# Kernel optimization log

Measured on AMD Instinct MI355X. Metric: run time of the kernel, lower is better.

## Reference

```python
import jax, jax.numpy as jnp
import numpy as np

LAYERS = 5      # lstm_layers
H = 1           # lstm_hidden_size
IN = 21         # 9 (rot) + 6 (v) + 6 (u)
NEG = 0.1       # LeakyReLU negative slope
EPS = 1e-5      # BatchNorm1d eps


def _lstm_cell(x, h, c, w_ih, w_hh):
    # torch gate order: i, f, g, o ; no biases (lstm_bias=False)
    gates = x @ w_ih.T + h @ w_hh.T              # [k, 4H]
    i, f, g, o = jnp.split(gates, 4, axis=-1)
    i = jax.nn.sigmoid(i)
    f = jax.nn.sigmoid(f)
    g = jnp.tanh(g)
    o = jax.nn.sigmoid(o)
    c_new = f * c + i * g
    h_new = o * jnp.tanh(c_new)
    return h_new, c_new


def _bn_train(z, gamma, beta):
    # BatchNorm1d in training mode: batch stats, biased variance
    m = z.mean(axis=0)
    var = z.var(axis=0)
    return gamma * (z - m) / jnp.sqrt(var + EPS) + beta


def setup_inputs() -> dict:
    key = jax.random.key(0)
    ks = jax.random.split(key, 14)
    k, T = 65536, 32
    s = 0.2  # init scale, roughly torch uniform(-1/sqrt(H)) magnitude
    inp = {
        "r": jax.random.normal(ks[0], (k, T, 9), jnp.float32),
        "v": jax.random.normal(ks[1], (k, T, 6), jnp.float32),
        "u": jax.random.normal(ks[2], (k, T, 6), jnp.float32),
        # LSTM weights: layer 0 sees IN features, layers 1..4 see H
        "w_ih0": jax.random.normal(ks[3], (4 * H, IN), jnp.float32) * s,
        "w_ih_rest": jax.random.normal(ks[4], (LAYERS - 1, 4 * H, H), jnp.float32) * s,
        "w_hh": jax.random.normal(ks[5], (LAYERS, 4 * H, H), jnp.float32) * s,
        # FC head: Linear(H,32,no bias) -> BN -> LReLU -> Linear(32,32) -> BN -> LReLU -> Linear(32,6)
        "W1": jax.random.normal(ks[6], (32, H), jnp.float32) * s,
        "g1": jnp.ones((32,), jnp.float32),
        "b1": jnp.zeros((32,), jnp.float32),
        "W2": jax.random.normal(ks[7], (32, 32), jnp.float32) * s,
        "g2": jnp.ones((32,), jnp.float32),
        "b2": jnp.zeros((32,), jnp.float32),
        "W3": jax.random.normal(ks[8], (6, 32), jnp.float32) * s,
    }
    return inp


def reference(r, v, u, w_ih0, w_ih_rest, w_hh, W1, g1, b1, W2, g2, b2, W3):
    x = jnp.concatenate([r, v, u], axis=-1)          # [k, T, 21]
    k = x.shape[0]
    h0 = jnp.zeros((LAYERS, k, H), x.dtype)
    c0 = jnp.zeros((LAYERS, k, H), x.dtype)
    xs = jnp.swapaxes(x, 0, 1)                       # [T, k, 21]

    def step(carry, xt):
        h, c = carry
        hs, cs = [], []
        layer_in = xt
        for l in range(LAYERS):
            w_ih = w_ih0 if l == 0 else w_ih_rest[l - 1]
            hl, cl = _lstm_cell(layer_in, h[l], c[l], w_ih, w_hh[l])
            hs.append(hl)
            cs.append(cl)
            layer_in = hl
        return (jnp.stack(hs), jnp.stack(cs)), layer_in  # top-layer output

    (hT, cT), outs = jax.lax.scan(step, (h0, c0), xs)    # outs: [T, k, H]

    # fc applied to out[:, 0] -> first timestep of top layer
    y = outs[0]                                          # [k, H]
    y = jax.nn.leaky_relu(_bn_train(y @ W1.T, g1, b1), NEG)
    y = jax.nn.leaky_relu(_bn_train(y @ W2.T, g2, b2), NEG)
    dv = y @ W3.T                                        # [k, 6]
    return dv[:, None], hT, cT
```

## Files before the change

### kernel.cpp

```cpp
#include <hip/hip_runtime.h>
#include <hip/hip_fp16.h>
#include <math.h>

#define T 32
#define NEGS 0.1f
#define EPS 1e-5f
#define NREG 33
#define NH (3 * NREG)


__device__ __forceinline__ float rcp_fast(float x) { return __builtin_amdgcn_rcpf(x); }
__device__ __forceinline__ float sigm(float x) { return rcp_fast(1.0f + __expf(-x)); }
__device__ __forceinline__ float tanh_fast(float x) {
    float t = __expf(2.0f * fabsf(x));
    float r = 1.0f - 2.0f * rcp_fast(t + 1.0f);
    return copysignf(r, x);
}
__device__ __forceinline__ float lrelu(float x) { return x > 0.0f ? x : NEGS * x; }

__device__ __forceinline__ void bn1_ab(const float* __restrict__ W1,
                                       const float* __restrict__ g1,
                                       const float* __restrict__ b1,
                                       float my, float vy, int j,
                                       float& a, float& b, float& tau, int& flip)
{
    float wj = W1[j];
    a = g1[j] * wj * rsqrtf(fmaf(wj * wj, vy, EPS));
    b = b1[j];
    if (a > 0.0f)      { tau = my - b / a; flip = 0; }
    else if (a < 0.0f) { tau = my - b / a; flip = 1; }
    else               { tau = (b > 0.0f ? -__builtin_inff() : __builtin_inff()); flip = 0; }
}

__device__ __forceinline__ void reduce_stats(const double* __restrict__ bSums, int nb, int k,
                                             float* outMy, float* outVy)
{
    const int tid = threadIdx.x;
    double sy = 0.0, sq = 0.0;
    for (int i = tid; i < nb; i += 256) { sy += bSums[2 * i]; sq += bSums[2 * i + 1]; }
#pragma unroll
    for (int off = 32; off; off >>= 1) {
        sy += __shfl_down(sy, off);
        sq += __shfl_down(sq, off);
    }
    __shared__ double dS[4], dQ[4];
    const int wid = tid >> 6, lane = tid & 63;
    if (lane == 0) { dS[wid] = sy; dQ[wid] = sq; }
    __syncthreads();
    if (tid == 0) {
        double tS = dS[0] + dS[1] + dS[2] + dS[3];
        double tQ = dQ[0] + dQ[1] + dQ[2] + dQ[3];
        float my = (float)(tS / k);
        *outMy = my;
        *outVy = (float)(tQ / k) - my * my;
    }
    __syncthreads();
}

__global__ __launch_bounds__(256)
void gates_kernel(const float* __restrict__ r, const float* __restrict__ v,
                  const float* __restrict__ u, const float* __restrict__ wih0,
                  ushort4* __restrict__ xg, int k)
{
    const int idx = blockIdx.x * 256 + threadIdx.x;
    const int s = idx >> 5, t = idx & 31;

    float wi0[4][21];
#pragma unroll
    for (int g = 0; g < 4; ++g)
#pragma unroll
        for (int j = 0; j < 21; ++j) wi0[g][j] = wih0[g * 21 + j];

    const float* rp = r + (size_t)s * 288 + t * 9;
    const float* vp = v + (size_t)s * 192 + t * 6;
    const float* up = u + (size_t)s * 192 + t * 6;
    float x[21];
#pragma unroll
    for (int j = 0; j < 9; ++j) x[j] = rp[j];
#pragma unroll
    for (int j = 0; j < 6; ++j) x[9 + j] = vp[j];
#pragma unroll
    for (int j = 0; j < 6; ++j) x[15 + j] = up[j];

    float acc[4];
#pragma unroll
    for (int g = 0; g < 4; ++g) {
        float a = 0.f;
#pragma unroll
        for (int j = 0; j < 21; ++j) a = fmaf(wi0[g][j], x[j], a);
        acc[g] = a;
    }
    ushort4 pk;
    pk.x = __half_as_ushort(__float2half(acc[0]));
    pk.y = __half_as_ushort(__float2half(acc[1]));
    pk.z = __half_as_ushort(__float2half(acc[2]));
    pk.w = __half_as_ushort(__float2half(acc[3]));
    xg[idx] = pk;
}

__global__ __launch_bounds__(256, 1)
void recur_kernel(const ushort4* __restrict__ xg, const float* __restrict__ wihr,
                  const float* __restrict__ whhp, float* __restrict__ out,
                  double* __restrict__ bSums, float* __restrict__ wsy, int k)
{
    const int s = blockIdx.x * 256 + threadIdx.x;

    float wir[4][4];
#pragma unroll
    for (int l = 0; l < 4; ++l)
#pragma unroll
        for (int g = 0; g < 4; ++g) wir[l][g] = wihr[l * 4 + g];
    float whh[5][4];
#pragma unroll
    for (int l = 0; l < 5; ++l)
#pragma unroll
        for (int g = 0; g < 4; ++g) whh[l][g] = whhp[l * 4 + g];

    ushort4 gbuf[T];
    const ushort4* gp = xg + (size_t)s * T;
#pragma unroll
    for (int t = 0; t < T; ++t) gbuf[t] = gp[t];

    float h[5] = {0.f, 0.f, 0.f, 0.f, 0.f};
    float c[5] = {0.f, 0.f, 0.f, 0.f, 0.f};
    float y0 = 0.f;

#pragma unroll
    for (int t = 0; t < T; ++t) {
        const ushort4 G = gbuf[t];
        float a0 = fmaf(whh[0][0], h[0], __half2float(__ushort_as_half(G.x)));
        float a1 = fmaf(whh[0][1], h[0], __half2float(__ushort_as_half(G.y)));
        float a2 = fmaf(whh[0][2], h[0], __half2float(__ushort_as_half(G.z)));
        float a3 = fmaf(whh[0][3], h[0], __half2float(__ushort_as_half(G.w)));
        {
            float ii = sigm(a0), ff = sigm(a1);
            float gg = tanh_fast(a2), oo = sigm(a3);
            c[0] = ff * c[0] + ii * gg;
            h[0] = oo * tanh_fast(c[0]);
        }
        float xin = h[0];
#pragma unroll
        for (int l = 1; l < 5; ++l) {
            float b0 = fmaf(wir[l - 1][0], xin, whh[l][0] * h[l]);
            float b1 = fmaf(wir[l - 1][1], xin, whh[l][1] * h[l]);
            float b2 = fmaf(wir[l - 1][2], xin, whh[l][2] * h[l]);
            float b3 = fmaf(wir[l - 1][3], xin, whh[l][3] * h[l]);
            float ii = sigm(b0), ff = sigm(b1);
            float gg = tanh_fast(b2), oo = sigm(b3);
            c[l] = ff * c[l] + ii * gg;
            h[l] = oo * tanh_fast(c[l]);
            xin = h[l];
        }
        if (t == 0) y0 = h[4];
    }

#pragma unroll
    for (int l = 0; l < 5; ++l) {
        out[(size_t)6 * k + (size_t)l * k + s] = h[l];
        out[(size_t)11 * k + (size_t)l * k + s] = c[l];
    }
    wsy[s] = y0;

    float ys = y0, yq = y0 * y0;
#pragma unroll
    for (int off = 32; off; off >>= 1) {
        ys += __shfl_down(ys, off);
        yq += __shfl_down(yq, off);
    }
    __shared__ float pS[4], pQ[4];
    const int wid = threadIdx.x >> 6, lane = threadIdx.x & 63;
    if (lane == 0) { pS[wid] = ys; pQ[wid] = yq; }
    __syncthreads();
    if (threadIdx.x == 0) {
        bSums[2 * blockIdx.x] = (double)(pS[0] + pS[1] + pS[2] + pS[3]);
        bSums[2 * blockIdx.x + 1] = (double)(pQ[0] + pQ[1] + pQ[2] + pQ[3]);
    }
}

__global__ __launch_bounds__(256, 1)
void lstm_fused(const float* __restrict__ r, const float* __restrict__ v,
                const float* __restrict__ u,
                const float* __restrict__ wih0, const float* __restrict__ wihr,
                const float* __restrict__ whhp,
                float* __restrict__ out, double* __restrict__ bSums,
                float* __restrict__ wsy, int k)
{
    const int s = blockIdx.x * 256 + threadIdx.x;
    float wi0[4][21];
#pragma unroll
    for (int g = 0; g < 4; ++g)
#pragma unroll
        for (int j = 0; j < 21; ++j) wi0[g][j] = wih0[g * 21 + j];
    float wir[4][4];
#pragma unroll
    for (int l = 0; l < 4; ++l)
#pragma unroll
        for (int g = 0; g < 4; ++g) wir[l][g] = wihr[l * 4 + g];
    float whh[5][4];
#pragma unroll
    for (int l = 0; l < 5; ++l)
#pragma unroll
        for (int g = 0; g < 4; ++g) whh[l][g] = whhp[l * 4 + g];

    const float4* r4 = reinterpret_cast<const float4*>(r + (size_t)s * (T * 9));
    const float4* v4 = reinterpret_cast<const float4*>(v + (size_t)s * (T * 6));
    const float4* u4 = reinterpret_cast<const float4*>(u + (size_t)s * (T * 6));

    float h[5] = {0.f, 0.f, 0.f, 0.f, 0.f};
    float c[5] = {0.f, 0.f, 0.f, 0.f, 0.f};
    float y0 = 0.f;

    for (int t0 = 0; t0 < T; t0 += 4) {
        const int cb = t0 >> 2;
        float4 rb[9], vb[6], ub[6];
#pragma unroll
        for (int q = 0; q < 9; ++q) rb[q] = r4[cb * 9 + q];
#pragma unroll
        for (int q = 0; q < 6; ++q) vb[q] = v4[cb * 6 + q];
#pragma unroll
        for (int q = 0; q < 6; ++q) ub[q] = u4[cb * 6 + q];
        float rf[36], vf[24], uf[24];
#pragma unroll
        for (int q = 0; q < 9; ++q) {
            rf[4 * q] = rb[q].x; rf[4 * q + 1] = rb[q].y;
            rf[4 * q + 2] = rb[q].z; rf[4 * q + 3] = rb[q].w;
        }
#pragma unroll
        for (int q = 0; q < 6; ++q) {
            vf[4 * q] = vb[q].x; vf[4 * q + 1] = vb[q].y;
            vf[4 * q + 2] = vb[q].z; vf[4 * q + 3] = vb[q].w;
            uf[4 * q] = ub[q].x; uf[4 * q + 1] = ub[q].y;
            uf[4 * q + 2] = ub[q].z; uf[4 * q + 3] = ub[q].w;
        }
#pragma unroll
        for (int dt = 0; dt < 4; ++dt) {
            float x[21];
#pragma unroll
            for (int j = 0; j < 9; ++j) x[j] = rf[dt * 9 + j];
#pragma unroll
            for (int j = 0; j < 6; ++j) x[9 + j] = vf[dt * 6 + j];
#pragma unroll
            for (int j = 0; j < 6; ++j) x[15 + j] = uf[dt * 6 + j];
            float gt[4];
#pragma unroll
            for (int g = 0; g < 4; ++g) {
                float a = whh[0][g] * h[0];
#pragma unroll
                for (int j = 0; j < 21; ++j) a = fmaf(wi0[g][j], x[j], a);
                gt[g] = a;
            }
            {
                float ii = sigm(gt[0]), ff = sigm(gt[1]);
                float gg = tanh_fast(gt[2]), oo = sigm(gt[3]);
                c[0] = ff * c[0] + ii * gg;
                h[0] = oo * tanh_fast(c[0]);
            }
            float xin = h[0];
#pragma unroll
            for (int l = 1; l < 5; ++l) {
                float b0 = fmaf(wir[l - 1][0], xin, whh[l][0] * h[l]);
                float b1 = fmaf(wir[l - 1][1], xin, whh[l][1] * h[l]);
                float b2 = fmaf(wir[l - 1][2], xin, whh[l][2] * h[l]);
                float b3 = fmaf(wir[l - 1][3], xin, whh[l][3] * h[l]);
                float ii = sigm(b0), ff = sigm(b1);
                float gg = tanh_fast(b2), oo = sigm(b3);
                c[l] = ff * c[l] + ii * gg;
                h[l] = oo * tanh_fast(c[l]);
                xin = h[l];
            }
            if (t0 + dt == 0) y0 = h[4];
        }
    }
#pragma unroll
    for (int l = 0; l < 5; ++l) {
        out[(size_t)6 * k + (size_t)l * k + s] = h[l];
        out[(size_t)11 * k + (size_t)l * k + s] = c[l];
    }
    wsy[s] = y0;
    float ys = y0, yq = y0 * y0;
#pragma unroll
    for (int off = 32; off; off >>= 1) {
        ys += __shfl_down(ys, off);
        yq += __shfl_down(yq, off);
    }
    __shared__ float pS[4], pQ[4];
    const int wid = threadIdx.x >> 6, lane = threadIdx.x & 63;
    if (lane == 0) { pS[wid] = ys; pQ[wid] = yq; }
    __syncthreads();
    if (threadIdx.x == 0) {
        bSums[2 * blockIdx.x] = (double)(pS[0] + pS[1] + pS[2] + pS[3]);
        bSums[2 * blockIdx.x + 1] = (double)(pQ[0] + pQ[1] + pQ[2] + pQ[3]);
    }
}

__global__ __launch_bounds__(256)
void hist_kernel(const float* __restrict__ W1, const float* __restrict__ g1,
                 const float* __restrict__ b1, const double* __restrict__ bSums, int nb,
                 float* __restrict__ bHist, const float* __restrict__ wsy, int k)
{
    __shared__ float sMy, sVy;
    __shared__ float sTau[32];
    __shared__ float sH[NH];
    const int tid = threadIdx.x;
    reduce_stats(bSums, nb, k, &sMy, &sVy);
    if (tid < NH) sH[tid] = 0.f;
    if (tid < 32) {
        float a, b, tau; int flip;
        bn1_ab(W1, g1, b1, sMy, sVy, tid, a, b, tau, flip);
        sTau[tid] = tau;
    }
    __syncthreads();
    const float my = sMy;
    const int stride = gridDim.x * 256;
    for (int s = blockIdx.x * 256 + tid; s < k; s += stride) {
        const float y = wsy[s];
        const float yc = y - my;
        int rgn = 0;
#pragma unroll
        for (int j = 0; j < 32; ++j) rgn += (y > sTau[j]) ? 1 : 0;
        atomicAdd(&sH[rgn], 1.0f);
        atomicAdd(&sH[NREG + rgn], yc);
        atomicAdd(&sH[2 * NREG + rgn], yc * yc);
    }
    __syncthreads();
    if (tid < NH) bHist[blockIdx.x * NH + tid] = sH[tid];
}

__global__ __launch_bounds__(256)
void tables_kernel(const float* __restrict__ W1, const float* __restrict__ g1,
                   const float* __restrict__ b1, const float* __restrict__ W2,
                   const float* __restrict__ g2, const float* __restrict__ b2,
                   const double* __restrict__ bSums, int nb,
                   const float* __restrict__ bHist, int nhb,
                   float* __restrict__ gPQ, int k)
{
    __shared__ float sMy, sVy;
    __shared__ float sA[32], sB[32], sTau[32];
    __shared__ int sRank[32], sFlip[32];
    __shared__ float sS0[NREG], sS1[NREG], sS2[NREG];
    __shared__ float sW2[1024];
    __shared__ float sSumY1[32];
    __shared__ float sM[1024];
    __shared__ float sI2[32], sM2v[32], sB2[32];
    const int tid = threadIdx.x;

    reduce_stats(bSums, nb, k, &sMy, &sVy);
    for (int i = tid; i < 1024; i += 256) sW2[i] = W2[i];
    if (tid < NH) {
        float acc = 0.f;
        for (int bk = 0; bk < nhb; ++bk) acc += bHist[bk * NH + tid];
        if (tid < NREG)           sS0[tid] = acc;
        else if (tid < 2 * NREG)  sS1[tid - NREG] = acc;
        else                      sS2[tid - 2 * NREG] = acc;
    }
    if (tid < 32) {
        float a, b, tau; int flip;
        bn1_ab(W1, g1, b1, sMy, sVy, tid, a, b, tau, flip);
        sA[tid] = a; sB[tid] = b; sTau[tid] = tau; sFlip[tid] = flip;
        sB2[tid] = b2[tid];
    }
    __syncthreads();
    if (tid < 32) {
        int rk = 0;
        float tj = sTau[tid];
#pragma unroll
        for (int l = 0; l < 32; ++l)
            rk += (sTau[l] < tj || (sTau[l] == tj && l < tid)) ? 1 : 0;
        sRank[tid] = rk;
    }
    __syncthreads();
    if (tid < 32) {
        const int rk = sRank[tid], fl = sFlip[tid];
        const float a = sA[tid], b = sB[tid];
        float acc = 0.f;
        for (int rg = 0; rg < NREG; ++rg) {
            float m = (((rk < rg) ? 1 : 0) != fl) ? 1.0f : NEGS;
            acc += m * (a * sS1[rg] + b * sS0[rg]);
        }
        sSumY1[tid] = acc;
    }
    for (int p = tid; p < 1024; p += 256) {
        const int j = p >> 5, l = p & 31;
        const int rj = sRank[j], fj = sFlip[j];
        const int rl = sRank[l], flp = sFlip[l];
        const float aj = sA[j], bj = sB[j], al = sA[l], bl = sB[l];
        const float caa = aj * al, cab = aj * bl + al * bj, cbb = bj * bl;
        float acc = 0.f;
        for (int rg = 0; rg < NREG; ++rg) {
            float mj = (((rj < rg) ? 1 : 0) != fj) ? 1.0f : NEGS;
            float ml = (((rl < rg) ? 1 : 0) != flp) ? 1.0f : NEGS;
            acc += mj * ml * (caa * sS2[rg] + cab * sS1[rg] + cbb * sS0[rg]);
        }
        sM[p] = acc;
    }
    __syncthreads();
    if (tid < 32) {
        const int i = tid;
        float s2 = 0.f, ss2 = 0.f;
#pragma unroll
        for (int j = 0; j < 32; ++j) {
            float wij = sW2[i * 32 + j];
            s2 = fmaf(wij, sSumY1[j], s2);
            float tj = 0.f;
#pragma unroll
            for (int l = 0; l < 32; ++l) tj = fmaf(sW2[i * 32 + l], sM[j * 32 + l], tj);
            ss2 = fmaf(wij, tj, ss2);
        }
        float m2 = s2 / k;
        float v2 = ss2 / k - m2 * m2;
        sM2v[i] = m2;
        sI2[i] = g2[i] * rsqrtf(v2 + EPS);
    }
    __syncthreads();
    for (int idx = tid; idx < NREG * 32; idx += 256) {
        const int rg = idx >> 5, i = idx & 31;
        float Ai = 0.f, Bi = 0.f;
#pragma unroll
        for (int j = 0; j < 32; ++j) {
            float m = (((sRank[j] < rg) ? 1 : 0) != sFlip[j]) ? 1.0f : NEGS;
            float w = sW2[i * 32 + j] * m;
            Ai = fmaf(w, sA[j], Ai);
            Bi = fmaf(w, sB[j], Bi);
        }
        gPQ[idx] = sI2[i] * Ai;
        gPQ[NREG * 32 + idx] = sI2[i] * (Bi - sM2v[i]) + sB2[i];
    }
    if (tid < 32) gPQ[2 * NREG * 32 + tid] = sTau[tid];
    if (tid == 0) gPQ[2 * NREG * 32 + 32] = sMy;
}

__global__ __launch_bounds__(256)
void final_kernel(const float* __restrict__ W3, const float* __restrict__ wsy,
                  const float* __restrict__ gPQ, float* __restrict__ out, int k)
{
    __shared__ float sTau[32], sW3[192], sMy;
    __shared__ float sP[NREG][33], sQ[NREG][33];
    const int tid = threadIdx.x;
    for (int idx = tid; idx < NREG * 32; idx += 256) {
        const int rg = idx >> 5, i = idx & 31;
        sP[rg][i] = gPQ[idx];
        sQ[rg][i] = gPQ[NREG * 32 + idx];
    }
    if (tid < 192) sW3[tid] = W3[tid];
    if (tid < 32) sTau[tid] = gPQ[2 * NREG * 32 + tid];
    if (tid == 0) sMy = gPQ[2 * NREG * 32 + 32];
    __syncthreads();
    const int s = blockIdx.x * 256 + tid;
    const float y = wsy[s];
    const float yc = y - sMy;
    int rgn = 0;
#pragma unroll
    for (int j = 0; j < 32; ++j) rgn += (y > sTau[j]) ? 1 : 0;
    float dv[6] = {0.f, 0.f, 0.f, 0.f, 0.f, 0.f};
#pragma unroll
    for (int i = 0; i < 32; ++i) {
        float y2 = lrelu(fmaf(sP[rgn][i], yc, sQ[rgn][i]));
#pragma unroll
        for (int m = 0; m < 6; ++m) dv[m] = fmaf(sW3[m * 32 + i], y2, dv[m]);
    }
#pragma unroll
    for (int m = 0; m < 6; ++m) out[(size_t)s * 6 + m] = dv[m];
}

extern "C" void kernel_launch(void* const* d_in, const int* in_sizes, int n_in,
                              void* d_out, int out_size, void* d_ws, size_t ws_size,
                              hipStream_t stream)
{
    const float* r    = (const float*)d_in[0];
    const float* v    = (const float*)d_in[1];
    const float* u    = (const float*)d_in[2];
    const float* wih0 = (const float*)d_in[3];
    const float* wihr = (const float*)d_in[4];
    const float* whhp = (const float*)d_in[5];
    const float* W1   = (const float*)d_in[6];
    const float* g1v  = (const float*)d_in[7];
    const float* b1v  = (const float*)d_in[8];
    const float* W2   = (const float*)d_in[9];
    const float* g2v  = (const float*)d_in[10];
    const float* b2v  = (const float*)d_in[11];
    const float* W3   = (const float*)d_in[12];

    const int k = in_sizes[0] / (T * 9);
    const int blocks = k / 256;
    const int HB = 64;
    float* out = (float*)d_out;

    double* bSums = (double*)d_ws;
    float* bHist  = (float*)((char*)d_ws + 4096);
    float* wsy    = (float*)((char*)d_ws + 32768);
    const size_t xg_off = 32768 + (size_t)k * 4;
    const size_t need = xg_off + (size_t)k * T * 8 + 2176 * 4;

    float* gPQ;
    if (ws_size >= need) {
        ushort4* xg = (ushort4*)((char*)d_ws + xg_off);
        gPQ = (float*)((char*)d_ws + xg_off + (size_t)k * T * 8);
        gates_kernel<<<(k * T) / 256, 256, 0, stream>>>(r, v, u, wih0, xg, k);
        recur_kernel<<<blocks, 256, 0, stream>>>(xg, wihr, whhp, out, bSums, wsy, k);
    } else {
        gPQ = (float*)((char*)d_ws + xg_off);
        lstm_fused<<<blocks, 256, 0, stream>>>(r, v, u, wih0, wihr, whhp, out, bSums, wsy, k);
    }
    hist_kernel<<<HB, 256, 0, stream>>>(W1, g1v, b1v, bSums, blocks, bHist, wsy, k);
    tables_kernel<<<1, 256, 0, stream>>>(W1, g1v, b1v, W2, g2v, b2v, bSums, blocks,
                                         bHist, HB, gPQ, k);
    final_kernel<<<blocks, 256, 0, stream>>>(W3, wsy, gPQ, out, k);
}
```

Baseline: 266.4 us.

## Stage gate inputs through LDS and transpose xg to time-major layout

The gates kernel now loads each block's r/v/u input rows with coalesced float4 reads into shared memory. It computes the gate preactivations from there and writes xg transposed to a [T][k] layout through a shared-memory buffer. The recurrence kernel then reads xg per timestep with coalesced accesses instead of each thread reading a 256-byte strided row. This costs extra shared memory and a block barrier in the gates kernel.

After: 270.8 us. About the same (+1.6%).

```diff
diff --git a/kernel.cpp b/kernel.cpp
--- a/kernel.cpp
+++ b/kernel.cpp
@@ -62,8 +62,11 @@
                   const float* __restrict__ u, const float* __restrict__ wih0,
                   ushort4* __restrict__ xg, int k)
 {
-    const int idx = blockIdx.x * 256 + threadIdx.x;
-    const int s = idx >> 5, t = idx & 31;
+    __shared__ float inS[4 * 1344];
+    __shared__ ushort4 gbuf[8 * 33];
+    const int tid = threadIdx.x;
+    const int w = tid >> 6, lane = tid & 63;
+    const int s0 = blockIdx.x * 8;
 
     float wi0[4][21];
 #pragma unroll
@@ -71,16 +74,30 @@
 #pragma unroll
         for (int j = 0; j < 21; ++j) wi0[g][j] = wih0[g * 21 + j];
 
-    const float* rp = r + (size_t)s * 288 + t * 9;
-    const float* vp = v + (size_t)s * 192 + t * 6;
-    const float* up = u + (size_t)s * 192 + t * 6;
+    {
+        const int sw = s0 + 2 * w;
+        const float4* rG = (const float4*)(r + (size_t)sw * 288);
+        const float4* vG = (const float4*)(v + (size_t)sw * 192);
+        const float4* uG = (const float4*)(u + (size_t)sw * 192);
+        float4* wS = ((float4*)inS) + w * 336;
+#pragma unroll
+        for (int it = 0; it < 6; ++it) {
+            int i = lane + it * 64;
+            if (i < 336) {
+                float4 val = (i < 144) ? rG[i] : (i < 240 ? vG[i - 144] : uG[i - 240]);
+                wS[i] = val;
+            }
+        }
+    }
+    const int sl = (lane >> 5), t = lane & 31;
+    const float* base = inS + w * 1344;
     float x[21];
 #pragma unroll
-    for (int j = 0; j < 9; ++j) x[j] = rp[j];
-#pragma unroll
-    for (int j = 0; j < 6; ++j) x[9 + j] = vp[j];
-#pragma unroll
-    for (int j = 0; j < 6; ++j) x[15 + j] = up[j];
+    for (int j = 0; j < 9; ++j) x[j] = base[sl * 288 + t * 9 + j];
+#pragma unroll
+    for (int j = 0; j < 6; ++j) x[9 + j] = base[576 + sl * 192 + t * 6 + j];
+#pragma unroll
+    for (int j = 0; j < 6; ++j) x[15 + j] = base[960 + sl * 192 + t * 6 + j];
 
     float acc[4];
 #pragma unroll
@@ -95,7 +112,13 @@
     pk.y = __half_as_ushort(__float2half(acc[1]));
     pk.z = __half_as_ushort(__float2half(acc[2]));
     pk.w = __half_as_ushort(__float2half(acc[3]));
-    xg[idx] = pk;
+
+    const int sblk = 2 * w + sl;
+    gbuf[sblk * 33 + t] = pk;
+    __syncthreads();
+
+    const int tS = tid >> 3, sS = tid & 7;
+    xg[(size_t)tS * k + s0 + sS] = gbuf[sS * 33 + tS];
 }
 
 __global__ __launch_bounds__(256, 1)
@@ -117,9 +140,8 @@
         for (int g = 0; g < 4; ++g) whh[l][g] = whhp[l * 4 + g];
 
     ushort4 gbuf[T];
-    const ushort4* gp = xg + (size_t)s * T;
-#pragma unroll
-    for (int t = 0; t < T; ++t) gbuf[t] = gp[t];
+#pragma unroll
+    for (int t = 0; t < T; ++t) gbuf[t] = xg[(size_t)t * k + s];
 
     float h[5] = {0.f, 0.f, 0.f, 0.f, 0.f};
     float c[5] = {0.f, 0.f, 0.f, 0.f, 0.f};
@@ -495,7 +517,7 @@
     if (ws_size >= need) {
         ushort4* xg = (ushort4*)((char*)d_ws + xg_off);
         gPQ = (float*)((char*)d_ws + xg_off + (size_t)k * T * 8);
-        gates_kernel<<<(k * T) / 256, 256, 0, stream>>>(r, v, u, wih0, xg, k);
+        gates_kernel<<<k / 8, 256, 0, stream>>>(r, v, u, wih0, xg, k);
         recur_kernel<<<blocks, 256, 0, stream>>>(xg, wihr, whhp, out, bSums, wsy, k);
     } else {
         gPQ = (float*)((char*)d_ws + xg_off);
```
